# Kernel tuning notes

Hardware: AMD Instinct MI355X
Metric: run time of the kernel (lower is better)

The kernel has to match this reference:

```python
import jax, jax.numpy as jnp
import numpy as np

EPS_F = 1e-12
M, N = 64, 4096  # feature dim m, num nodes n


def setup_inputs() -> dict:
    key = jax.random.key(0)
    k1, k2, k3, k4 = jax.random.split(key, 4)
    # X: (m, n) node features transposed, as in the repo (features.t())
    X = jax.random.normal(k1, (M, N), dtype=jnp.float32)
    # F: (m, m) parameter, xavier_uniform init
    bound = float(np.sqrt(6.0 / (M + M)))
    F = jax.random.uniform(k2, (M, M), minval=-bound, maxval=bound, dtype=jnp.float32)
    # Q_S: (n, n) orthogonal eigenvector matrix of the (symmetric, normalized) adjacency
    A = jax.random.normal(k3, (N, N), dtype=jnp.float32)
    Q_S, _ = jnp.linalg.qr(A)
    Q_S = Q_S.astype(jnp.float32)
    # Lambda_S: (n, 1) eigenvalues of normalized adjacency, inside (-1, 1)
    Lambda_S = jnp.sort(
        jax.random.uniform(k4, (N, 1), minval=-0.95, maxval=0.95, dtype=jnp.float32), axis=0
    )
    gamma = jnp.asarray(0.8, dtype=jnp.float32)
    return {"X": X, "F": F, "Q_S": Q_S, "Lambda_S": Lambda_S, "gamma": gamma}


def reference(X, F, Q_S, Lambda_S, gamma):
    # g(F) = F^T F / (||F^T F||_F + eps)  -- Frobenius-normalized Gram matrix
    FF = F.T @ F                                   # (m, m)
    G_F = FF / (jnp.linalg.norm(FF) + EPS_F)       # (m, m), symmetric PSD, ||.||_F ~ 1
    # spectral decomposition of g(F)
    Lambda_F, Q_F = jnp.linalg.eigh(G_F)           # (m,), (m, m)
    # closed-form equilibrium of Z = gamma * g(F) Z S^T + X in the joint eigenbasis
    D = 1.0 / (1.0 - gamma * Lambda_F[:, None] * Lambda_S.reshape(1, -1))  # (m, n)
    Z = Q_F @ (D * (Q_F.T @ X @ Q_S)) @ Q_S.T      # (m, n)
    return Z
```

## Files before the change

kernel.cpp:

```cpp
#include <hip/hip_runtime.h>
#include <math.h>


typedef short short8 __attribute__((ext_vector_type(8)));
typedef float floatx16 __attribute__((ext_vector_type(16)));

#define KSPLIT 8
#define KCHUNK 512
constexpr int Mdim = 64;
constexpr int Ndim = 4096;

__device__ inline ushort f2bf(float f) {
    uint u = __float_as_uint(f);
    u += 0x7fff + ((u >> 16) & 1);
    return (ushort)(u >> 16);
}
__device__ inline float bf2f(ushort h) { return __uint_as_float(((uint)h) << 16); }

__device__ inline floatx16 mfma_bf16(short8 a, short8 b, floatx16 c) {
    return __builtin_amdgcn_mfma_f32_32x32x16_bf16(a, b, c, 0, 0, 0);
}

struct SharedGemm { ushort Ah[4096], Al[4096], Bh[4096], Bl[4096]; };
struct SharedPrep { float Fraw[64 * 65]; ushort Ph[4096], Pl[4096]; float red[256]; };
union SharedU { SharedGemm g; SharedPrep p; };

__global__ __launch_bounds__(256) void init_kernel(float* __restrict__ W, float* __restrict__ Z) {
    const int i = blockIdx.x * 256 + threadIdx.x;
    float4 z = {0.f, 0.f, 0.f, 0.f};
    if (i < 65536) *(float4*)&W[i * 4] = z;
    else *(float4*)&Z[(i - 65536) * 4] = z;
}

__device__ void prep_body(SharedPrep& sp, const float* __restrict__ F, float* __restrict__ Gout) {
    const int t = threadIdx.x;
    const int l = t & 63, w = t >> 6;
    const int tm = w & 1, tn = w >> 1;
    const int am = tm * 32 + (l & 31);
    const int bn = tn * 32 + (l & 31);
    const int lk = l >> 5;

    for (int s = 0; s < 4; ++s) {
        int e = t + 256 * s;
        int r = e >> 4, q = (e & 15) * 4;
        float4 v = *(const float4*)&F[r * 64 + q];
        float fa[4] = {v.x, v.y, v.z, v.w};
        for (int i = 0; i < 4; ++i) sp.Fraw[r * 65 + q + i] = fa[i];
    }
    __syncthreads();
    {
        int c = t >> 2, kbase = (t & 3) * 16;
        ushort hh[16], ll[16];
#pragma unroll
        for (int kk = 0; kk < 16; ++kk) {
            float v = sp.Fraw[(kbase + kk) * 65 + c];
            ushort h = f2bf(v);
            hh[kk] = h;
            ll[kk] = f2bf(v - bf2f(h));
        }
#pragma unroll
        for (int g = 0; g < 2; ++g) {
            int gk = (kbase >> 3) + g;
            int idx = c * 64 + ((gk ^ (c & 7)) * 8);
#pragma unroll
            for (int u = 0; u < 8; ++u) { sp.Ph[idx + u] = hh[8 * g + u]; sp.Pl[idx + u] = ll[8 * g + u]; }
        }
    }
    __syncthreads();
    floatx16 acc;
    for (int i = 0; i < 16; ++i) acc[i] = 0.f;
    for (int s16 = 0; s16 < 4; ++s16) {
        int gk = 2 * s16 + lk;
        int ai = am * 64 + ((gk ^ (am & 7)) * 8);
        int bi = bn * 64 + ((gk ^ (bn & 7)) * 8);
        short8 ah = *(const short8*)&sp.Ph[ai];
        short8 al = *(const short8*)&sp.Pl[ai];
        short8 bh = *(const short8*)&sp.Ph[bi];
        short8 bl = *(const short8*)&sp.Pl[bi];
        acc = mfma_bf16(ah, bh, acc);
        acc = mfma_bf16(al, bh, acc);
        acc = mfma_bf16(ah, bl, acc);
    }
    float ss = 0.f;
    for (int r = 0; r < 16; ++r) ss += acc[r] * acc[r];
    sp.red[t] = ss;
    __syncthreads();
    for (int off = 128; off > 0; off >>= 1) {
        if (t < off) sp.red[t] += sp.red[t + off];
        __syncthreads();
    }
    const float inv = 1.0f / (sqrtf(sp.red[0]) + 1e-12f);
    for (int r = 0; r < 16; ++r) {
        int row = (r & 3) + 8 * (r >> 2) + 4 * lk + tm * 32;
        int col = tn * 32 + (l & 31);
        float v = acc[r] * inv;
        Gout[row * 64 + col] = v;
        ushort h = f2bf(v);
        int idx = row * 64 + (((col >> 3) ^ (row & 7)) * 8 + (col & 7));
        sp.Ph[idx] = h;
        sp.Pl[idx] = f2bf(v - bf2f(h));
    }
    for (int j = 1; j < 5; ++j) {
        __syncthreads();
        floatx16 a2;
        for (int i = 0; i < 16; ++i) a2[i] = 0.f;
        for (int s16 = 0; s16 < 4; ++s16) {
            int gk = 2 * s16 + lk;
            int ai = am * 64 + ((gk ^ (am & 7)) * 8);
            int bi = bn * 64 + ((gk ^ (bn & 7)) * 8);
            short8 ah = *(const short8*)&sp.Ph[ai];
            short8 al = *(const short8*)&sp.Pl[ai];
            short8 bh = *(const short8*)&sp.Ph[bi];
            short8 bl = *(const short8*)&sp.Pl[bi];
            a2 = mfma_bf16(ah, bh, a2);
            a2 = mfma_bf16(al, bh, a2);
            a2 = mfma_bf16(ah, bl, a2);
        }
        __syncthreads();
        for (int r = 0; r < 16; ++r) {
            int row = (r & 3) + 8 * (r >> 2) + 4 * lk + tm * 32;
            int col = tn * 32 + (l & 31);
            float v = a2[r];
            Gout[j * 4096 + row * 64 + col] = v;
            ushort h = f2bf(v);
            int idx = row * 64 + (((col >> 3) ^ (row & 7)) * 8 + (col & 7));
            sp.Ph[idx] = h;
            sp.Pl[idx] = f2bf(v - bf2f(h));
        }
    }
}

template <bool TB, bool DOPREP>
__global__ __launch_bounds__(256, 4) void gemm_kernel(const float* __restrict__ A,
                                                      const float* __restrict__ Bm,
                                                      float* __restrict__ C,
                                                      const float* __restrict__ F,
                                                      float* __restrict__ Gp) {
    __shared__ SharedU sh;
    const int bid = blockIdx.x;
    if (DOPREP) {
        if (bid == 0) { prep_body(sh.p, F, Gp); return; }
    }
    const int b = DOPREP ? bid - 1 : bid;
    const int n0 = (b & 63) * 64;
    const int kb = (b >> 6) * KCHUNK;
    const int t = threadIdx.x;
    const int l = t & 63, w = t >> 6;
    const int tm = w & 1, tn = w >> 1;
    const int am = tm * 32 + (l & 31);
    const int bn = tn * 32 + (l & 31);
    const int lk = l >> 5;
    const int sr = t >> 2, sj = t & 3;
    const int nq = t & 15, kr2 = 2 * (t >> 4);

    floatx16 acc;
    for (int i = 0; i < 16; ++i) acc[i] = 0.f;

    for (int step = 0; step < KCHUNK / 64; ++step) {
        const int k0 = kb + step * 64;
        float4 av[4], bv[4], bva[2], bvb[2];
        for (int s = 0; s < 4; ++s)
            av[s] = *(const float4*)&A[sr * 4096 + k0 + 4 * sj + 16 * s];
        if (TB) {
            for (int s = 0; s < 4; ++s)
                bv[s] = *(const float4*)&Bm[(size_t)(n0 + sr) * 4096 + k0 + 4 * sj + 16 * s];
        } else {
            for (int s = 0; s < 2; ++s) {
                bva[s] = *(const float4*)&Bm[(size_t)(k0 + kr2 + 32 * s) * 4096 + n0 + 4 * nq];
                bvb[s] = *(const float4*)&Bm[(size_t)(k0 + kr2 + 1 + 32 * s) * 4096 + n0 + 4 * nq];
            }
        }
        __syncthreads();
        for (int s = 0; s < 4; ++s) {
            int off = 4 * sj + 16 * s;
            int idx = sr * 64 + (((off >> 3) ^ (sr & 7)) * 8 + (off & 7));
            float fa[4] = {av[s].x, av[s].y, av[s].z, av[s].w};
            ushort4 h4, l4;
            ushort* hp = (ushort*)&h4; ushort* lp = (ushort*)&l4;
            for (int i = 0; i < 4; ++i) {
                ushort h = f2bf(fa[i]);
                hp[i] = h; lp[i] = f2bf(fa[i] - bf2f(h));
            }
            *(ushort4*)&sh.g.Ah[idx] = h4;
            *(ushort4*)&sh.g.Al[idx] = l4;
        }
        if (TB) {
            for (int s = 0; s < 4; ++s) {
                int off = 4 * sj + 16 * s;
                int idx = sr * 64 + (((off >> 3) ^ (sr & 7)) * 8 + (off & 7));
                float fb[4] = {bv[s].x, bv[s].y, bv[s].z, bv[s].w};
                ushort4 h4, l4;
                ushort* hp = (ushort*)&h4; ushort* lp = (ushort*)&l4;
                for (int i = 0; i < 4; ++i) {
                    ushort h = f2bf(fb[i]);
                    hp[i] = h; lp[i] = f2bf(fb[i] - bf2f(h));
                }
                *(ushort4*)&sh.g.Bh[idx] = h4;
                *(ushort4*)&sh.g.Bl[idx] = l4;
            }
        } else {
            for (int s = 0; s < 2; ++s) {
                int k = kr2 + 32 * s;
                float fa[4] = {bva[s].x, bva[s].y, bva[s].z, bva[s].w};
                float fb[4] = {bvb[s].x, bvb[s].y, bvb[s].z, bvb[s].w};
                for (int i = 0; i < 4; ++i) {
                    int n = 4 * nq + i;
                    int idx = n * 64 + (((k >> 3) ^ (n & 7)) * 8 + (k & 7));
                    ushort2 hp2, lp2;
                    hp2.x = f2bf(fa[i]); hp2.y = f2bf(fb[i]);
                    lp2.x = f2bf(fa[i] - bf2f(hp2.x));
                    lp2.y = f2bf(fb[i] - bf2f(hp2.y));
                    *(ushort2*)&sh.g.Bh[idx] = hp2;
                    *(ushort2*)&sh.g.Bl[idx] = lp2;
                }
            }
        }
        __syncthreads();
#pragma unroll
        for (int s16 = 0; s16 < 4; ++s16) {
            int gk = 2 * s16 + lk;
            int ai = am * 64 + ((gk ^ (am & 7)) * 8);
            int bi = bn * 64 + ((gk ^ (bn & 7)) * 8);
            short8 ah = *(const short8*)&sh.g.Ah[ai];
            short8 al = *(const short8*)&sh.g.Al[ai];
            short8 bh = *(const short8*)&sh.g.Bh[bi];
            short8 bl = *(const short8*)&sh.g.Bl[bi];
            acc = mfma_bf16(ah, bh, acc);
            acc = mfma_bf16(al, bh, acc);
            acc = mfma_bf16(ah, bl, acc);
        }
    }
    const int colg = n0 + tn * 32 + (l & 31);
#pragma unroll
    for (int r = 0; r < 16; ++r) {
        int row = (r & 3) + 8 * (r >> 2) + 4 * lk + tm * 32;
        atomicAdd(&C[row * 4096 + colg], acc[r]);
    }
}

__global__ __launch_bounds__(256) void solve_kernel(const float* __restrict__ W,
                                                    const float* __restrict__ Gp,
                                                    const float* __restrict__ lam,
                                                    const float* __restrict__ gammap,
                                                    float* __restrict__ Y) {
    __shared__ float Gs[64][68];
    __shared__ float T[64][17];
    const int t = threadIdx.x;
    const int c0 = blockIdx.x * 16;
    for (int e = t; e < 1024; e += 256)
        T[e >> 4][e & 15] = W[(e >> 4) * 4096 + c0 + (e & 15)];
    const int tx = t & 15;
    const int r4 = (t >> 4) * 4;
    const float a = gammap[0] * lam[c0 + tx];
    float s = a;
    for (int j = 0; j < 5; ++j) {
        __syncthreads();
        for (int e = t; e < 4096; e += 256) Gs[e >> 6][e & 63] = Gp[j * 4096 + e];
        __syncthreads();
        float u0 = 0.f, u1 = 0.f, u2 = 0.f, u3 = 0.f;
#pragma unroll 8
        for (int k = 0; k < 64; ++k) {
            const float tv = T[k][tx];
            const float4 g = *(const float4*)&Gs[k][r4];
            u0 += g.x * tv; u1 += g.y * tv; u2 += g.z * tv; u3 += g.w * tv;
        }
        __syncthreads();
        T[r4 + 0][tx] += s * u0;
        T[r4 + 1][tx] += s * u1;
        T[r4 + 2][tx] += s * u2;
        T[r4 + 3][tx] += s * u3;
        s = s * s;
    }
    __syncthreads();
    for (int e = t; e < 1024; e += 256)
        Y[(e >> 4) * 4096 + c0 + (e & 15)] = T[e >> 4][e & 15];
}

extern "C" void kernel_launch(void* const* d_in, const int* in_sizes, int n_in,
                              void* d_out, int out_size, void* d_ws, size_t ws_size,
                              hipStream_t stream) {
    const float* X     = (const float*)d_in[0];
    const float* F     = (const float*)d_in[1];
    const float* Qs    = (const float*)d_in[2];
    const float* lam   = (const float*)d_in[3];
    const float* gamma = (const float*)d_in[4];
    float* Z = (float*)d_out;

    float* W  = (float*)d_ws;
    float* Y  = W + Mdim * Ndim;
    float* Gp = Y + Mdim * Ndim;

    init_kernel<<<512, 256, 0, stream>>>(W, Z);
    gemm_kernel<false, true><<<64 * KSPLIT + 1, 256, 0, stream>>>(X, Qs, W, F, Gp);
    solve_kernel<<<Ndim / 16, 256, 0, stream>>>(W, Gp, lam, gamma, Y);
    gemm_kernel<true, false><<<64 * KSPLIT, 256, 0, stream>>>(Y, Qs, Z, nullptr, nullptr);
}
```

Before: 169.2 us.

## Drop B low-part bf16 split, double-buffer B loads, and double K-split

The GEMM kernel no longer keeps a bf16 low-order residual for the B operand (Q_S), so each step issues two MFMAs instead of three and one fewer LDS array is written and read. B tiles are now prefetched one step ahead into a register double buffer so global loads overlap the conversion and MFMA work. KSPLIT goes from 8 to 16 with half the K chunk, giving more blocks but more atomic adds into C. Dropping the B residual lowers accuracy to roughly bf16 precision on Q_S, which may break tolerance.

```diff
diff --git a/kernel.cpp b/kernel.cpp
--- a/kernel.cpp
+++ b/kernel.cpp
@@ -5,8 +5,8 @@
 typedef short short8 __attribute__((ext_vector_type(8)));
 typedef float floatx16 __attribute__((ext_vector_type(16)));
 
-#define KSPLIT 8
-#define KCHUNK 512
+#define KSPLIT 16
+#define KCHUNK 256
 constexpr int Mdim = 64;
 constexpr int Ndim = 4096;
 
@@ -21,7 +21,7 @@
     return __builtin_amdgcn_mfma_f32_32x32x16_bf16(a, b, c, 0, 0, 0);
 }
 
-struct SharedGemm { ushort Ah[4096], Al[4096], Bh[4096], Bl[4096]; };
+struct SharedGemm { ushort Ah[4096], Al[4096], Bh[4096]; };
 struct SharedPrep { float Fraw[64 * 65]; ushort Ph[4096], Pl[4096]; float red[256]; };
 union SharedU { SharedGemm g; SharedPrep p; };
 
@@ -156,64 +156,85 @@
     floatx16 acc;
     for (int i = 0; i < 16; ++i) acc[i] = 0.f;
 
+    float4 bbuf[2][4];
+    if (TB) {
+#pragma unroll
+        for (int s = 0; s < 4; ++s)
+            bbuf[0][s] = *(const float4*)&Bm[(size_t)(n0 + sr) * 4096 + kb + 4 * sj + 16 * s];
+    } else {
+#pragma unroll
+        for (int s = 0; s < 2; ++s) {
+            bbuf[0][2 * s + 0] = *(const float4*)&Bm[(size_t)(kb + kr2 + 32 * s) * 4096 + n0 + 4 * nq];
+            bbuf[0][2 * s + 1] = *(const float4*)&Bm[(size_t)(kb + kr2 + 1 + 32 * s) * 4096 + n0 + 4 * nq];
+        }
+    }
+
+#pragma unroll
     for (int step = 0; step < KCHUNK / 64; ++step) {
         const int k0 = kb + step * 64;
-        float4 av[4], bv[4], bva[2], bvb[2];
+        const int cur = step & 1, nxt = cur ^ 1;
+        float4 av[4];
+#pragma unroll
         for (int s = 0; s < 4; ++s)
             av[s] = *(const float4*)&A[sr * 4096 + k0 + 4 * sj + 16 * s];
+        __syncthreads();
+        if (step + 1 < KCHUNK / 64) {
+            const int k1 = k0 + 64;
+            if (TB) {
+#pragma unroll
+                for (int s = 0; s < 4; ++s)
+                    bbuf[nxt][s] = *(const float4*)&Bm[(size_t)(n0 + sr) * 4096 + k1 + 4 * sj + 16 * s];
+            } else {
+#pragma unroll
+                for (int s = 0; s < 2; ++s) {
+                    bbuf[nxt][2 * s + 0] = *(const float4*)&Bm[(size_t)(k1 + kr2 + 32 * s) * 4096 + n0 + 4 * nq];
+                    bbuf[nxt][2 * s + 1] = *(const float4*)&Bm[(size_t)(k1 + kr2 + 1 + 32 * s) * 4096 + n0 + 4 * nq];
+                }
+            }
+        }
         if (TB) {
-            for (int s = 0; s < 4; ++s)
-                bv[s] = *(const float4*)&Bm[(size_t)(n0 + sr) * 4096 + k0 + 4 * sj + 16 * s];
+#pragma unroll
+            for (int s = 0; s < 4; ++s) {
+                int off = 4 * sj + 16 * s;
+                int idx = sr * 64 + (((off >> 3) ^ (sr & 7)) * 8 + (off & 7));
+                float fb[4] = {bbuf[cur][s].x, bbuf[cur][s].y, bbuf[cur][s].z, bbuf[cur][s].w};
+                ushort4 h4;
+                ushort* hp = (ushort*)&h4;
+#pragma unroll
+                for (int i = 0; i < 4; ++i) hp[i] = f2bf(fb[i]);
+                *(ushort4*)&sh.g.Bh[idx] = h4;
+            }
         } else {
+#pragma unroll
             for (int s = 0; s < 2; ++s) {
-                bva[s] = *(const float4*)&Bm[(size_t)(k0 + kr2 + 32 * s) * 4096 + n0 + 4 * nq];
-                bvb[s] = *(const float4*)&Bm[(size_t)(k0 + kr2 + 1 + 32 * s) * 4096 + n0 + 4 * nq];
+                int k = kr2 + 32 * s;
+                float fa[4] = {bbuf[cur][2 * s].x, bbuf[cur][2 * s].y, bbuf[cur][2 * s].z, bbuf[cur][2 * s].w};
+                float fb[4] = {bbuf[cur][2 * s + 1].x, bbuf[cur][2 * s + 1].y, bbuf[cur][2 * s + 1].z, bbuf[cur][2 * s + 1].w};
+#pragma unroll
+                for (int i = 0; i < 4; ++i) {
+                    int n = 4 * nq + i;
+                    int idx = n * 64 + (((k >> 3) ^ (n & 7)) * 8 + (k & 7));
+                    ushort2 hp2;
+                    hp2.x = f2bf(fa[i]);
+                    hp2.y = f2bf(fb[i]);
+                    *(ushort2*)&sh.g.Bh[idx] = hp2;
+                }
             }
         }
-        __syncthreads();
+#pragma unroll
         for (int s = 0; s < 4; ++s) {
             int off = 4 * sj + 16 * s;
             int idx = sr * 64 + (((off >> 3) ^ (sr & 7)) * 8 + (off & 7));
             float fa[4] = {av[s].x, av[s].y, av[s].z, av[s].w};
             ushort4 h4, l4;
             ushort* hp = (ushort*)&h4; ushort* lp = (ushort*)&l4;
+#pragma unroll
             for (int i = 0; i < 4; ++i) {
                 ushort h = f2bf(fa[i]);
                 hp[i] = h; lp[i] = f2bf(fa[i] - bf2f(h));
             }
             *(ushort4*)&sh.g.Ah[idx] = h4;
             *(ushort4*)&sh.g.Al[idx] = l4;
-        }
-        if (TB) {
-            for (int s = 0; s < 4; ++s) {
-                int off = 4 * sj + 16 * s;
-                int idx = sr * 64 + (((off >> 3) ^ (sr & 7)) * 8 + (off & 7));
-                float fb[4] = {bv[s].x, bv[s].y, bv[s].z, bv[s].w};
-                ushort4 h4, l4;
-                ushort* hp = (ushort*)&h4; ushort* lp = (ushort*)&l4;
-                for (int i = 0; i < 4; ++i) {
-                    ushort h = f2bf(fb[i]);
-                    hp[i] = h; lp[i] = f2bf(fb[i] - bf2f(h));
-                }
-                *(ushort4*)&sh.g.Bh[idx] = h4;
-                *(ushort4*)&sh.g.Bl[idx] = l4;
-            }
-        } else {
-            for (int s = 0; s < 2; ++s) {
-                int k = kr2 + 32 * s;
-                float fa[4] = {bva[s].x, bva[s].y, bva[s].z, bva[s].w};
-                float fb[4] = {bvb[s].x, bvb[s].y, bvb[s].z, bvb[s].w};
-                for (int i = 0; i < 4; ++i) {
-                    int n = 4 * nq + i;
-                    int idx = n * 64 + (((k >> 3) ^ (n & 7)) * 8 + (k & 7));
-                    ushort2 hp2, lp2;
-                    hp2.x = f2bf(fa[i]); hp2.y = f2bf(fb[i]);
-                    lp2.x = f2bf(fa[i] - bf2f(hp2.x));
-                    lp2.y = f2bf(fb[i] - bf2f(hp2.y));
-                    *(ushort2*)&sh.g.Bh[idx] = hp2;
-                    *(ushort2*)&sh.g.Bl[idx] = lp2;
-                }
-            }
         }
         __syncthreads();
 #pragma unroll
@@ -224,10 +245,8 @@
             short8 ah = *(const short8*)&sh.g.Ah[ai];
             short8 al = *(const short8*)&sh.g.Al[ai];
             short8 bh = *(const short8*)&sh.g.Bh[bi];
-            short8 bl = *(const short8*)&sh.g.Bl[bi];
             acc = mfma_bf16(ah, bh, acc);
             acc = mfma_bf16(al, bh, acc);
-            acc = mfma_bf16(ah, bl, acc);
         }
     }
     const int colg = n0 + tn * 32 + (l & 31);
```

Measured after the change: 158.1 us. 6.6% less time.
